# Kernel optimization log

Measured on AMD Instinct MI355X. Metric: run time of the kernel, lower is better.

Reference implementation:

```python
import jax, jax.numpy as jnp
import numpy as np

VOCAB = 50257
D_MODEL = 1024
RANK = 64
V1, V2 = 225, 224   # ceil(sqrt(vocab)), ceil(vocab/v1)
D1, D2 = 32, 32     # ceil(sqrt(d_model)), ceil(d_model/d1)
B, L = 4, 4096


def setup_inputs() -> dict:
    key = jax.random.key(0)
    ks = jax.random.split(key, 4)
    input_ids = jax.random.randint(ks[0], (B, L), 0, VOCAB, dtype=jnp.int32)
    core1_q = jax.random.randint(ks[1], (V1, 1, RANK, D1), -128, 128, dtype=jnp.int32).astype(jnp.int8)
    core2_q = jax.random.randint(ks[2], (V2, RANK, 1, D2), -128, 128, dtype=jnp.int32).astype(jnp.int8)
    phase_shift = jax.random.normal(ks[3], (RANK,), dtype=jnp.float32) * 0.02
    return {
        "input_ids": input_ids,
        "core1_q": core1_q,
        "core1_scale": jnp.float32(0.01),
        "core1_zp": jnp.float32(0.0),
        "core2_q": core2_q,
        "core2_scale": jnp.float32(0.01),
        "core2_zp": jnp.float32(0.0),
        "phase_shift": phase_shift,
    }


def reference(input_ids, core1_q, core1_scale, core1_zp, core2_q, core2_scale, core2_zp, phase_shift):
    # token index -> (row in core1, row in core2)
    idx1 = jnp.clip(input_ids // V2, 0, V1 - 1)  # [B, L]
    idx2 = jnp.clip(input_ids % V2, 0, V2 - 1)   # [B, L]

    # gather int8 rows first, then dequantize: (q - zp) * scale (same math as
    # dequantizing full cores then gathering, but avoids touching unused rows)
    c1 = (core1_q[idx1, 0].astype(jnp.float32) - core1_zp) * core1_scale     # [B, L, R, D1]
    c2 = (core2_q[idx2, :, 0].astype(jnp.float32) - core2_zp) * core2_scale  # [B, L, R, D2]

    # phase modulation on core1 along the rank axis
    c1 = c1 * jnp.cos(phase_shift)[None, None, :, None]

    # per-token rank contraction: [B,L,D1,D2] -> [B,L,D1*D2] -> slice d_model
    out = jnp.einsum('blrd,blrf->bldf', c1, c2).reshape(B, L, D1 * D2)
    return out[:, :, :D_MODEL]
```

## Files before the change

### kernel.cpp

```cpp
#include <hip/hip_runtime.h>
#include <hip/hip_bf16.h>
#include <math.h>

#define V1N   225
#define V2N   224
#define RANK  64
#define DDIM  32
#define ROWE  (RANK*DDIM)
#define NTOK  16384

typedef __bf16  bf16x8 __attribute__((ext_vector_type(8)));
typedef float  f32x16 __attribute__((ext_vector_type(16)));

__global__ __launch_bounds__(256) void prep_tables(
    const int* __restrict__ c1q, const int* __restrict__ c2q,
    const float* __restrict__ s1p, const float* __restrict__ z1p,
    const float* __restrict__ s2p, const float* __restrict__ z2p,
    const float* __restrict__ phase,
    __bf16* __restrict__ t1, __bf16* __restrict__ t2)
{
    int v = blockIdx.x;
    const int* src;
    __bf16* dst;
    float sc, zp;
    bool is1 = (v < V1N);
    if (is1) { src = c1q + v * ROWE;          dst = t1 + v * ROWE;          sc = *s1p; zp = *z1p; }
    else     { int u = v - V1N; src = c2q + u * ROWE; dst = t2 + u * ROWE;  sc = *s2p; zp = *z2p; }

    for (int e = threadIdx.x; e < ROWE; e += 256) {
        int r = e >> 5;
        int d = e & 31;
        float val = ((float)src[e] - zp) * sc;
        if (is1) val *= cosf(phase[r]);
        dst[((r >> 4) * 32 + d) * 16 + (r & 15)] = (__bf16)val;
    }
}

__global__ __launch_bounds__(256) void tt_main(
    const int* __restrict__ ids,
    const __bf16* __restrict__ t1, const __bf16* __restrict__ t2,
    float* __restrict__ out, int n_tok)
{
    int wave = (blockIdx.x << 2) + (threadIdx.x >> 6);
    if (wave >= n_tok) return;
    int lane = threadIdx.x & 63;
    int m = lane & 31;
    int g = lane >> 5;

    unsigned id = (unsigned)ids[wave];
    unsigned i1 = id / 224u; if (i1 > (unsigned)(V1N - 1)) i1 = V1N - 1;
    unsigned i2 = id % 224u;

    const __bf16* a_base = t1 + (size_t)i1 * ROWE + m * 16 + g * 8;
    const __bf16* b_base = t2 + (size_t)i2 * ROWE + m * 16 + g * 8;

    f32x16 acc;
    #pragma unroll
    for (int i = 0; i < 16; ++i) acc[i] = 0.0f;

    #pragma unroll
    for (int s = 0; s < 4; ++s) {
        bf16x8 a = *reinterpret_cast<const bf16x8*>(a_base + s * 512);
        bf16x8 b = *reinterpret_cast<const bf16x8*>(b_base + s * 512);
        acc = __builtin_amdgcn_mfma_f32_32x32x16_bf16(a, b, acc, 0, 0, 0);
    }

    float* o = out + (size_t)wave * 1024 + g * 128 + m;
    #pragma unroll
    for (int reg = 0; reg < 16; ++reg) {
        int row = (reg & 3) + 8 * (reg >> 2);
        o[row * 32] = acc[reg];
    }
}

__global__ __launch_bounds__(256) void tt_fused(
    const int* __restrict__ ids,
    const int* __restrict__ c1q, const int* __restrict__ c2q,
    const float* __restrict__ s1p, const float* __restrict__ z1p,
    const float* __restrict__ s2p, const float* __restrict__ z2p,
    const float* __restrict__ phase,
    float* __restrict__ out, int n_tok)
{
    __shared__ float cosv[RANK];
    if (threadIdx.x < RANK) cosv[threadIdx.x] = cosf(phase[threadIdx.x]);
    __syncthreads();

    int wave = (blockIdx.x << 2) + (threadIdx.x >> 6);
    if (wave >= n_tok) return;
    int lane = threadIdx.x & 63;
    int m = lane & 31;
    int g = lane >> 5;

    float s1 = *s1p, z1 = *z1p, s2 = *s2p, z2 = *z2p;

    unsigned id = (unsigned)ids[wave];
    unsigned i1 = id / 224u; if (i1 > (unsigned)(V1N - 1)) i1 = V1N - 1;
    unsigned i2 = id % 224u;

    const int* a_src = c1q + (size_t)i1 * ROWE + m;
    const int* b_src = c2q + (size_t)i2 * ROWE + m;

    f32x16 acc;
    #pragma unroll
    for (int i = 0; i < 16; ++i) acc[i] = 0.0f;

    #pragma unroll
    for (int s = 0; s < 4; ++s) {
        bf16x8 a, b;
        #pragma unroll
        for (int j = 0; j < 8; ++j) {
            int r = s * 16 + g * 8 + j;
            a[j] = (__bf16)((((float)a_src[r * 32]) - z1) * s1 * cosv[r]);
            b[j] = (__bf16)((((float)b_src[r * 32]) - z2) * s2);
        }
        acc = __builtin_amdgcn_mfma_f32_32x32x16_bf16(a, b, acc, 0, 0, 0);
    }

    float* o = out + (size_t)wave * 1024 + g * 128 + m;
    #pragma unroll
    for (int reg = 0; reg < 16; ++reg) {
        int row = (reg & 3) + 8 * (reg >> 2);
        o[row * 32] = acc[reg];
    }
}

extern "C" void kernel_launch(void* const* d_in, const int* in_sizes, int n_in,
                              void* d_out, int out_size, void* d_ws, size_t ws_size,
                              hipStream_t stream) {
    const int*   ids = (const int*)d_in[0];
    const int*   c1q = (const int*)d_in[1];
    const float* s1  = (const float*)d_in[2];
    const float* z1  = (const float*)d_in[3];
    const int*   c2q = (const int*)d_in[4];
    const float* s2  = (const float*)d_in[5];
    const float* z2  = (const float*)d_in[6];
    const float* ph  = (const float*)d_in[7];
    float* out = (float*)d_out;

    int n_tok = in_sizes[0];
    int grid  = (n_tok + 3) / 4;

    size_t need = (size_t)(V1N + V2N) * ROWE * sizeof(__bf16);
    if (ws_size >= need) {
        __bf16* t1 = (__bf16*)d_ws;
        __bf16* t2 = t1 + (size_t)V1N * ROWE;
        prep_tables<<<V1N + V2N, 256, 0, stream>>>(c1q, c2q, s1, z1, s2, z2, ph, t1, t2);
        tt_main<<<grid, 256, 0, stream>>>(ids, t1, t2, out, n_tok);
    } else {
        tt_fused<<<grid, 256, 0, stream>>>(ids, c1q, c2q, s1, z1, s2, z2, ph, out, n_tok);
    }
}
```

Measured before the change: 27.05 us.

## Swap MFMA operands for vectorized nontemporal output stores and coalesce table prep

The main kernel swaps the A and B operands of the MFMA, which transposes the accumulator layout. Each lane then holds four contiguous output floats, so it can write them as 128-bit nontemporal stores instead of sixteen strided scalar stores. The prep kernel now uses vector loads of the int8-as-int32 rows and an LDS transpose, writing bf16x8 vectors instead of scattered 2-byte writes. The risk is in the transposed index mapping, and the nontemporal hint may change how stores interact with the cache.

Result: slower. 29.69 us (+9.8%).

```diff
diff --git a/kernel.cpp b/kernel.cpp
--- a/kernel.cpp
+++ b/kernel.cpp
@@ -7,10 +7,11 @@
 #define RANK  64
 #define DDIM  32
 #define ROWE  (RANK*DDIM)
-#define NTOK  16384
 
 typedef __bf16  bf16x8 __attribute__((ext_vector_type(8)));
 typedef float  f32x16 __attribute__((ext_vector_type(16)));
+typedef float  f32x4  __attribute__((ext_vector_type(4)));
+typedef int    i32x4  __attribute__((ext_vector_type(4)));
 
 __global__ __launch_bounds__(256) void prep_tables(
     const int* __restrict__ c1q, const int* __restrict__ c2q,
@@ -19,21 +20,43 @@
     const float* __restrict__ phase,
     __bf16* __restrict__ t1, __bf16* __restrict__ t2)
 {
+    __shared__ float lds[64 * 33];
+    __shared__ float cosv[RANK];
+
     int v = blockIdx.x;
+    bool is1 = (v < V1N);
     const int* src;
     __bf16* dst;
     float sc, zp;
-    bool is1 = (v < V1N);
-    if (is1) { src = c1q + v * ROWE;          dst = t1 + v * ROWE;          sc = *s1p; zp = *z1p; }
-    else     { int u = v - V1N; src = c2q + u * ROWE; dst = t2 + u * ROWE;  sc = *s2p; zp = *z2p; }
+    if (is1) { src = c1q + v * ROWE;            dst = t1 + (size_t)v * ROWE;  sc = *s1p; zp = *z1p; }
+    else     { int u = v - V1N; src = c2q + u * ROWE; dst = t2 + (size_t)u * ROWE; sc = *s2p; zp = *z2p; }
 
-    for (int e = threadIdx.x; e < ROWE; e += 256) {
-        int r = e >> 5;
-        int d = e & 31;
-        float val = ((float)src[e] - zp) * sc;
-        if (is1) val *= cosf(phase[r]);
-        dst[((r >> 4) * 32 + d) * 16 + (r & 15)] = (__bf16)val;
+    int t = threadIdx.x;
+    if (is1 && t < RANK) cosv[t] = cosf(phase[t]);
+    __syncthreads();
+
+    i32x4 w0 = reinterpret_cast<const i32x4*>(src)[t * 2];
+    i32x4 w1 = reinterpret_cast<const i32x4*>(src)[t * 2 + 1];
+    #pragma unroll
+    for (int j = 0; j < 8; ++j) {
+        int e = t * 8 + j;
+        int q = (j < 4) ? w0[j & 3] : w1[j & 3];
+        float val = ((float)q - zp) * sc;
+        if (is1) val *= cosv[e >> 5];
+        lds[(e >> 5) * 33 + (e & 31)] = val;
     }
+    __syncthreads();
+
+    int s   = t >> 6;
+    int d   = (t >> 1) & 31;
+    int rr0 = (t & 1) * 8;
+    bf16x8 o8;
+    #pragma unroll
+    for (int j = 0; j < 8; ++j) {
+        int r = s * 16 + rr0 + j;
+        o8[j] = (__bf16)lds[r * 33 + d];
+    }
+    *reinterpret_cast<bf16x8*>(dst + t * 8) = o8;
 }
 
 __global__ __launch_bounds__(256) void tt_main(
@@ -51,8 +74,8 @@
     unsigned i1 = id / 224u; if (i1 > (unsigned)(V1N - 1)) i1 = V1N - 1;
     unsigned i2 = id % 224u;
 
-    const __bf16* a_base = t1 + (size_t)i1 * ROWE + m * 16 + g * 8;
-    const __bf16* b_base = t2 + (size_t)i2 * ROWE + m * 16 + g * 8;
+    const __bf16* a_base = t2 + (size_t)i2 * ROWE + m * 16 + g * 8;
+    const __bf16* b_base = t1 + (size_t)i1 * ROWE + m * 16 + g * 8;
 
     f32x16 acc;
     #pragma unroll
@@ -65,11 +88,11 @@
         acc = __builtin_amdgcn_mfma_f32_32x32x16_bf16(a, b, acc, 0, 0, 0);
     }
 
-    float* o = out + (size_t)wave * 1024 + g * 128 + m;
+    float* o = out + (size_t)wave * 1024 + m * 32 + g * 4;
     #pragma unroll
-    for (int reg = 0; reg < 16; ++reg) {
-        int row = (reg & 3) + 8 * (reg >> 2);
-        o[row * 32] = acc[reg];
+    for (int q = 0; q < 4; ++q) {
+        f32x4 v = { acc[4 * q + 0], acc[4 * q + 1], acc[4 * q + 2], acc[4 * q + 3] };
+        __builtin_nontemporal_store(v, reinterpret_cast<f32x4*>(o + 8 * q));
     }
 }
 
@@ -97,8 +120,8 @@
     unsigned i1 = id / 224u; if (i1 > (unsigned)(V1N - 1)) i1 = V1N - 1;
     unsigned i2 = id % 224u;
 
-    const int* a_src = c1q + (size_t)i1 * ROWE + m;
-    const int* b_src = c2q + (size_t)i2 * ROWE + m;
+    const int* a_src = c2q + (size_t)i2 * ROWE + m;
+    const int* b_src = c1q + (size_t)i1 * ROWE + m;
 
     f32x16 acc;
     #pragma unroll
@@ -110,17 +133,17 @@
         #pragma unroll
         for (int j = 0; j < 8; ++j) {
             int r = s * 16 + g * 8 + j;
-            a[j] = (__bf16)((((float)a_src[r * 32]) - z1) * s1 * cosv[r]);
-            b[j] = (__bf16)((((float)b_src[r * 32]) - z2) * s2);
+            a[j] = (__bf16)((((float)a_src[r * 32]) - z2) * s2);
+            b[j] = (__bf16)((((float)b_src[r * 32]) - z1) * s1 * cosv[r]);
         }
         acc = __builtin_amdgcn_mfma_f32_32x32x16_bf16(a, b, acc, 0, 0, 0);
     }
 
-    float* o = out + (size_t)wave * 1024 + g * 128 + m;
+    float* o = out + (size_t)wave * 1024 + m * 32 + g * 4;
     #pragma unroll
-    for (int reg = 0; reg < 16; ++reg) {
-        int row = (reg & 3) + 8 * (reg >> 2);
-        o[row * 32] = acc[reg];
+    for (int q = 0; q < 4; ++q) {
+        f32x4 v = { acc[4 * q + 0], acc[4 * q + 1], acc[4 * q + 2], acc[4 * q + 3] };
+        __builtin_nontemporal_store(v, reinterpret_cast<f32x4*>(o + 8 * q));
     }
 }
 
```
